# Performance work log

Measured on AMD Instinct MI355X. Metric: run time of the kernel, lower is better.

Reference implementation:

```python
import jax, jax.numpy as jnp
import numpy as np

NDIM = 2
NSIG = 2
NCELLS = 1000
BATCH = 4
DT = 1e-3
NSTEPS = 251  # 1 + int((t1 - t0)/dt) with t0=0, t1=0.25
SIGMA = 1e-3


def _phi(y, pw1, pb1, pw2, pb2, pw3, pb3, pw4, pb4, pw5, pb5):
    # phi_nn: 2 -> 16 -> 32 -> 32 -> 16 -> 1 with tanh activations
    h = jnp.tanh(y @ pw1.T + pb1)
    h = jnp.tanh(h @ pw2.T + pb2)
    h = jnp.tanh(h @ pw3.T + pb3)
    h = jnp.tanh(h @ pw4.T + pb4)
    return h @ pw5.T + pb5  # (ncells, 1)


def setup_inputs() -> dict:
    key = jax.random.key(0)
    ks = jax.random.split(key, 16)
    # x = [t0, t1, y0.flat, tcrit, p0(2), p1(2)] per batch item
    y0 = 0.1 * jax.random.normal(ks[0], (BATCH, NCELLS, NDIM), dtype=jnp.float32)
    t0 = jnp.zeros((BATCH, 1), jnp.float32)
    t1 = jnp.full((BATCH, 1), 0.25, jnp.float32)
    tcrit = jnp.full((BATCH, 1), 0.125, jnp.float32)
    p0 = jax.random.normal(ks[1], (BATCH, 2), dtype=jnp.float32)
    p1 = jax.random.normal(ks[2], (BATCH, 2), dtype=jnp.float32)
    x = jnp.concatenate([t0, t1, y0.reshape(BATCH, -1), tcrit, p0, p1], axis=1)
    # Wiener increments ~ N(0, dt)
    dw = np.sqrt(DT).astype(np.float32) * jax.random.normal(
        ks[3], (BATCH, NSTEPS, NCELLS, NDIM), dtype=jnp.float32)
    # phi_nn weights (torch Linear: weight is (out, in)), init N(0, 0.1), bias 0
    def w(k, o, i):
        return 0.1 * jax.random.normal(k, (o, i), dtype=jnp.float32)
    inp = dict(x=x, dw=dw,
               pw1=w(ks[4], 16, 2), pb1=jnp.zeros(16, jnp.float32),
               pw2=w(ks[5], 32, 16), pb2=jnp.zeros(32, jnp.float32),
               pw3=w(ks[6], 32, 32), pb3=jnp.zeros(32, jnp.float32),
               pw4=w(ks[7], 16, 32), pb4=jnp.zeros(16, jnp.float32),
               pw5=w(ks[8], 1, 16), pb5=jnp.zeros(1, jnp.float32),
               tw=w(ks[9], NDIM, NSIG), tb=jnp.zeros(NDIM, jnp.float32))
    return inp


def reference(x, dw, pw1, pb1, pw2, pb2, pw3, pb3, pw4, pb4, pw5, pb5, tw, tb):
    phi_params = (pw1, pb1, pw2, pb2, pw3, pb3, pw4, pb4, pw5, pb5)
    grad_phi = jax.grad(lambda yy: jnp.sum(_phi(yy, *phi_params)))

    def simulate(xi, dwi):
        t0 = xi[0]
        y0 = xi[2:2 + NCELLS * NDIM].reshape(NCELLS, NDIM)
        ps = xi[2 + NCELLS * NDIM:]
        tcrit, p0, p1 = ps[0], ps[1:3], ps[3:5]
        ts = t0 + DT * jnp.arange(NSTEPS, dtype=xi.dtype)

        def step(y, t_dw):
            t, dwt = t_dw
            sig = jnp.where(t < tcrit, p0, p1)      # step signal f_signal(t, params)
            tilt = sig @ tw.T + tb                  # grad_tilt: (ndim,)
            drift = -(grad_phi(y) + tilt)           # f(t, y)
            y_new = y + drift * DT + SIGMA * dwt    # Euler-Maruyama
            return y_new, None

        y_final, _ = jax.lax.scan(step, y0, (ts, dwi))
        return y_final

    return jax.vmap(simulate)(x, dw)  # (BATCH, NCELLS, NDIM)
```

## Files before the change

kernel.cpp:

```cpp
#include <hip/hip_runtime.h>

#define NDIMC 2
#define NCELLS 1000
#define BATCHSZ 4
#define NSTEPS 251
#define XROW 2007

typedef float v2f __attribute__((ext_vector_type(2)));

__device__ __forceinline__ v2f pfma(v2f w, v2f v, v2f a) {
    return __builtin_elementwise_fma(w, v, a);
}

__device__ __forceinline__ float fast_tanh(float x) {
    float e = __builtin_amdgcn_exp2f(x * 2.885390081777926774f);
    float r = __builtin_amdgcn_rcpf(e + 1.0f);
    return fmaf(-2.0f, r, 1.0f);
}

template<int CTRL>
__device__ __forceinline__ float dpp_mov(float x) {
    return __int_as_float(__builtin_amdgcn_update_dpp(
        0, __float_as_int(x), CTRL, 0xf, 0xf, true));
}
template<int CTRL>
__device__ __forceinline__ float dpp_add(float z) { return z + dpp_mov<CTRL>(z); }

__device__ __forceinline__ float row16_sum(float z) {
    z = dpp_add<0xB1>(z);
    z = dpp_add<0x1B>(z);
    z = dpp_add<0x141>(z);
    z = dpp_add<0x140>(z);
    return z;
}

__device__ __forceinline__ float xor16(float z, bool odd) {
    float t = z, u = z;
    asm("v_permlane16_swap_b32 %0, %1" : "+v"(t), "+v"(u));
    return odd ? t : u;
}

struct G16 { v2f p[8]; };
__device__ __forceinline__ G16 gather16(float z) {
    G16 g;
    const float v0 = z;
    const float v1 = dpp_mov<0x4E>(v0);
    const float v2 = dpp_mov<0x141>(v0);
    const float v3 = dpp_mov<0x141>(v1);
    const float v4 = dpp_mov<0x140>(v0);
    const float v5 = dpp_mov<0x140>(v1);
    const float v6 = dpp_mov<0x140>(v2);
    const float v7 = dpp_mov<0x140>(v3);
    g.p[0] = v2f{v0, dpp_mov<0xB1>(v0)};
    g.p[1] = v2f{v1, dpp_mov<0xB1>(v1)};
    g.p[2] = v2f{v2, dpp_mov<0xB1>(v2)};
    g.p[3] = v2f{v3, dpp_mov<0xB1>(v3)};
    g.p[4] = v2f{v4, dpp_mov<0xB1>(v4)};
    g.p[5] = v2f{v5, dpp_mov<0xB1>(v5)};
    g.p[6] = v2f{v6, dpp_mov<0xB1>(v6)};
    g.p[7] = v2f{v7, dpp_mov<0xB1>(v7)};
    return g;
}

__device__ __forceinline__ float gdot16(const v2f (&w)[8], const G16& g, float bias) {
    v2f a0 = {bias, 0.f}, a1 = {0.f, 0.f}, a2 = {0.f, 0.f}, a3 = {0.f, 0.f};
    a0 = pfma(w[0], g.p[0], a0); a1 = pfma(w[1], g.p[1], a1);
    a2 = pfma(w[2], g.p[2], a2); a3 = pfma(w[3], g.p[3], a3);
    a0 = pfma(w[4], g.p[4], a0); a1 = pfma(w[5], g.p[5], a1);
    a2 = pfma(w[6], g.p[6], a2); a3 = pfma(w[7], g.p[7], a3);
    v2f s = (a0 + a1) + (a2 + a3);
    return s[0] + s[1];
}

__global__ __launch_bounds__(64, 2)
void phinn_sde_kernel(const float* __restrict__ x,   const float* __restrict__ dw,
                      const float* __restrict__ pw1, const float* __restrict__ pb1,
                      const float* __restrict__ pw2, const float* __restrict__ pb2,
                      const float* __restrict__ pw3, const float* __restrict__ pb3,
                      const float* __restrict__ pw4, const float* __restrict__ pb4,
                      const float* __restrict__ pw5, const float* __restrict__ pb5,
                      const float* __restrict__ tw,  const float* __restrict__ tb,
                      float* __restrict__ out)
{
    const int tid  = threadIdx.x;
    const int n    = tid & 31;
    const int s16  = n & 15;
    const int hi   = n >> 4;
    const bool odd = hi;
    const int np   = n ^ 16;
    const int rbk  = hi * 16;
    const int grp  = tid >> 5;
    const int b    = blockIdx.x / (NCELLS / 2);
    const int pair = blockIdx.x % (NCELLS / 2);
    const int cell = pair * 2 + grp;

    const int TAU[8] = {0, 2, 7, 5, 15, 13, 8, 10};

    const float r1a = pw1[s16 * 2 + 0];
    const float r1b = pw1[s16 * 2 + 1];
    const float rb1 = pb1[s16];
    const float rb2 = pb2[n];
    const float rb3 = pb3[n];
    const float rb4 = pb4[s16];
    const float rw5 = pw5[s16];

    v2f w2f[8], w3P[8], w3Q[8], w4f[8], w4b[8], w3bP[8], w3bQ[8], w2b[8];
    #pragma unroll
    for (int t = 0; t < 8; ++t) {
        const int j0 = s16 ^ TAU[t];
        const int j1 = j0 ^ 1;
        const int k0 = rbk + j0;
        const int k1 = rbk + j1;
        w2f[t]  = v2f{pw2[n * 16 + j0],   pw2[n * 16 + j1]};
        w3P[t]  = v2f{pw3[n * 32 + k0],   pw3[n * 32 + k1]};
        w3Q[t]  = v2f{pw3[np * 32 + k0],  pw3[np * 32 + k1]};
        w4f[t]  = v2f{pw4[s16 * 32 + k0], pw4[s16 * 32 + k1]};
        w4b[t]  = v2f{pw4[j0 * 32 + n],   pw4[j1 * 32 + n]};
        w3bP[t] = v2f{pw3[k0 * 32 + n],   pw3[k1 * 32 + n]};
        w3bQ[t] = v2f{pw3[k0 * 32 + np],  pw3[k1 * 32 + np]};
        w2b[t]  = v2f{pw2[k0 * 16 + s16], pw2[k1 * 16 + s16]};
    }

    const float* xb = x + (size_t)b * XROW;
    const float t0v    = xb[0];
    const float tcritv = xb[2 + NCELLS * NDIMC];
    const float p0x = xb[2003], p0y = xb[2004];
    const float p1x = xb[2005], p1y = xb[2006];
    const float tA0 = fmaf(p0x, tw[0], fmaf(p0y, tw[1], tb[0]));
    const float tA1 = fmaf(p0x, tw[2], fmaf(p0y, tw[3], tb[1]));
    const float tB0 = fmaf(p1x, tw[0], fmaf(p1y, tw[1], tb[0]));
    const float tB1 = fmaf(p1x, tw[2], fmaf(p1y, tw[3], tb[1]));

    float y0 = xb[2 + cell * 2 + 0];
    float y1 = xb[2 + cell * 2 + 1];

    const float* dwb = dw + (size_t)b * NSTEPS * NCELLS * NDIMC
                          + (size_t)pair * 2 * NDIMC;
    int dwoff = grp * NDIMC;

    #pragma unroll 1
    for (int i = 0; i < NSTEPS; ++i) {
        const float2 dwv = *(const float2*)(dwb + dwoff);
        dwoff += NCELLS * NDIMC;
        const float t = t0v + 0.001f * (float)i;

        const float h1 = fast_tanh(fmaf(r1a, y0, fmaf(r1b, y1, rb1)));

        const G16 G1 = gather16(h1);
        const float h2 = fast_tanh(gdot16(w2f, G1, rb2));

        const G16 G2 = gather16(h2);
        const float h3 = fast_tanh(gdot16(w3P, G2, rb3)
                                   + xor16(gdot16(w3Q, G2, 0.f), odd));

        const G16 G3 = gather16(h3);
        const float A4 = gdot16(w4f, G3, 0.f);
        const float h4 = fast_tanh(A4 + xor16(A4, odd) + rb4);

        const float g4p = rw5 * fmaf(-h4, h4, 1.0f);

        const G16 G4 = gather16(g4p);
        const float g3p = gdot16(w4b, G4, 0.f) * fmaf(-h3, h3, 1.0f);

        const G16 G5 = gather16(g3p);
        const float g2p = (gdot16(w3bP, G5, 0.f)
                           + xor16(gdot16(w3bQ, G5, 0.f), odd))
                          * fmaf(-h2, h2, 1.0f);

        const G16 G6 = gather16(g2p);
        const float A1 = gdot16(w2b, G6, 0.f);
        const float g1p = (A1 + xor16(A1, odd)) * fmaf(-h1, h1, 1.0f);

        const float v0 = row16_sum(r1a * g1p);
        const float v1 = row16_sum(r1b * g1p);

        const bool  cnd   = t < tcritv;
        const float tilt0 = cnd ? tA0 : tB0;
        const float tilt1 = cnd ? tA1 : tB1;
        y0 = fmaf(-0.001f, v0 + tilt0, fmaf(0.001f, dwv.x, y0));
        y1 = fmaf(-0.001f, v1 + tilt1, fmaf(0.001f, dwv.y, y1));
    }

    if (n == 0) {
        *(float2*)(out + ((size_t)b * NCELLS + cell) * NDIMC) = make_float2(y0, y1);
    }
}

extern "C" void kernel_launch(void* const* d_in, const int* in_sizes, int n_in,
                              void* d_out, int out_size, void* d_ws, size_t ws_size,
                              hipStream_t stream) {
    const float* x   = (const float*)d_in[0];
    const float* dw  = (const float*)d_in[1];
    const float* pw1 = (const float*)d_in[2];
    const float* pb1 = (const float*)d_in[3];
    const float* pw2 = (const float*)d_in[4];
    const float* pb2 = (const float*)d_in[5];
    const float* pw3 = (const float*)d_in[6];
    const float* pb3 = (const float*)d_in[7];
    const float* pw4 = (const float*)d_in[8];
    const float* pb4 = (const float*)d_in[9];
    const float* pw5 = (const float*)d_in[10];
    const float* pb5 = (const float*)d_in[11];
    const float* tw  = (const float*)d_in[12];
    const float* tb  = (const float*)d_in[13];
    float* out = (float*)d_out;

    dim3 grid(BATCHSZ * NCELLS / 2);
    dim3 block(64);
    phinn_sde_kernel<<<grid, block, 0, stream>>>(x, dw, pw1, pb1, pw2, pb2,
                                                 pw3, pb3, pw4, pb4, pw5, pb5,
                                                 tw, tb, out);
}
```

Before: 302.8 us.

## Exchange 32-wide layer activations through LDS broadcast instead of DPP gathers

The 32-wide layers (h2->h3, h3->h4, and the backward g3p->g2p, g2p->g1p) now stage their activations in shared memory. Each lane computes its full 32-term dot product from wide LDS broadcast reads, replacing the DPP gather trees and the permlane16 swap half-sums. The weights are reorganised into per-lane 16-pair register arrays to match. This removes many DPP moves and cross-half combines, but adds LDS round-trip latency on the serial critical path of every time step. There is no explicit barrier, so correctness relies on the 32 lanes of each group sitting in the same wavefront.

```diff
diff --git a/kernel.cpp b/kernel.cpp
--- a/kernel.cpp
+++ b/kernel.cpp
@@ -7,6 +7,10 @@
 #define XROW 2007
 
 typedef float v2f __attribute__((ext_vector_type(2)));
+typedef float v4f __attribute__((ext_vector_type(4)));
+
+__device__ __forceinline__ v2f vlo(v4f v) { return __builtin_shufflevector(v, v, 0, 1); }
+__device__ __forceinline__ v2f vhi(v4f v) { return __builtin_shufflevector(v, v, 2, 3); }
 
 __device__ __forceinline__ v2f pfma(v2f w, v2f v, v2f a) {
     return __builtin_elementwise_fma(w, v, a);
@@ -17,6 +21,7 @@
     float r = __builtin_amdgcn_rcpf(e + 1.0f);
     return fmaf(-2.0f, r, 1.0f);
 }
+
 
 template<int CTRL>
 __device__ __forceinline__ float dpp_mov(float x) {
@@ -32,12 +37,6 @@
     z = dpp_add<0x141>(z);
     z = dpp_add<0x140>(z);
     return z;
-}
-
-__device__ __forceinline__ float xor16(float z, bool odd) {
-    float t = z, u = z;
-    asm("v_permlane16_swap_b32 %0, %1" : "+v"(t), "+v"(u));
-    return odd ? t : u;
 }
 
 struct G16 { v2f p[8]; };
@@ -72,6 +71,23 @@
     return s[0] + s[1];
 }
 
+__device__ __forceinline__ float pdot32(const v2f (&w)[16], const float* p, float bias) {
+    v2f a0 = {bias, 0.f}, a1 = {0.f, 0.f}, a2 = {0.f, 0.f}, a3 = {0.f, 0.f};
+    #pragma unroll
+    for (int c = 0; c < 2; ++c) {
+        v4f u0 = *(const v4f*)(p + c * 16);
+        v4f u1 = *(const v4f*)(p + c * 16 + 4);
+        v4f u2 = *(const v4f*)(p + c * 16 + 8);
+        v4f u3 = *(const v4f*)(p + c * 16 + 12);
+        a0 = pfma(w[c*8+0], vlo(u0), a0); a1 = pfma(w[c*8+1], vhi(u0), a1);
+        a2 = pfma(w[c*8+2], vlo(u1), a2); a3 = pfma(w[c*8+3], vhi(u1), a3);
+        a0 = pfma(w[c*8+4], vlo(u2), a0); a1 = pfma(w[c*8+5], vhi(u2), a1);
+        a2 = pfma(w[c*8+6], vlo(u3), a2); a3 = pfma(w[c*8+7], vhi(u3), a3);
+    }
+    v2f s = (a0 + a1) + (a2 + a3);
+    return s[0] + s[1];
+}
+
 __global__ __launch_bounds__(64, 2)
 void phinn_sde_kernel(const float* __restrict__ x,   const float* __restrict__ dw,
                       const float* __restrict__ pw1, const float* __restrict__ pb1,
@@ -82,14 +98,12 @@
                       const float* __restrict__ tw,  const float* __restrict__ tb,
                       float* __restrict__ out)
 {
+    __shared__ __align__(16) float sh[2][4][32];
+
     const int tid  = threadIdx.x;
     const int n    = tid & 31;
+    const int grp  = tid >> 5;
     const int s16  = n & 15;
-    const int hi   = n >> 4;
-    const bool odd = hi;
-    const int np   = n ^ 16;
-    const int rbk  = hi * 16;
-    const int grp  = tid >> 5;
     const int b    = blockIdx.x / (NCELLS / 2);
     const int pair = blockIdx.x % (NCELLS / 2);
     const int cell = pair * 2 + grp;
@@ -104,22 +118,32 @@
     const float rb4 = pb4[s16];
     const float rw5 = pw5[s16];
 
-    v2f w2f[8], w3P[8], w3Q[8], w4f[8], w4b[8], w3bP[8], w3bQ[8], w2b[8];
+    v2f w2f[8], w4b[8];
     #pragma unroll
     for (int t = 0; t < 8; ++t) {
         const int j0 = s16 ^ TAU[t];
         const int j1 = j0 ^ 1;
-        const int k0 = rbk + j0;
-        const int k1 = rbk + j1;
-        w2f[t]  = v2f{pw2[n * 16 + j0],   pw2[n * 16 + j1]};
-        w3P[t]  = v2f{pw3[n * 32 + k0],   pw3[n * 32 + k1]};
-        w3Q[t]  = v2f{pw3[np * 32 + k0],  pw3[np * 32 + k1]};
-        w4f[t]  = v2f{pw4[s16 * 32 + k0], pw4[s16 * 32 + k1]};
-        w4b[t]  = v2f{pw4[j0 * 32 + n],   pw4[j1 * 32 + n]};
-        w3bP[t] = v2f{pw3[k0 * 32 + n],   pw3[k1 * 32 + n]};
-        w3bQ[t] = v2f{pw3[k0 * 32 + np],  pw3[k1 * 32 + np]};
-        w2b[t]  = v2f{pw2[k0 * 16 + s16], pw2[k1 * 16 + s16]};
-    }
+        w2f[t] = v2f{pw2[n * 16 + j0], pw2[n * 16 + j1]};
+        w4b[t] = v2f{pw4[j0 * 32 + n], pw4[j1 * 32 + n]};
+    }
+
+    v2f w3p[16];
+    #pragma unroll
+    for (int j = 0; j < 16; ++j) w3p[j] = ((const v2f*)pw3)[n * 16 + j];
+
+    v2f w4p[16];
+    #pragma unroll
+    for (int j = 0; j < 16; ++j) w4p[j] = ((const v2f*)pw4)[s16 * 16 + j];
+
+    v2f w3cp[16];
+    #pragma unroll
+    for (int j = 0; j < 16; ++j)
+        w3cp[j] = v2f{pw3[(2*j) * 32 + n], pw3[(2*j+1) * 32 + n]};
+
+    v2f w2cp[16];
+    #pragma unroll
+    for (int j = 0; j < 16; ++j)
+        w2cp[j] = v2f{pw2[(2*j) * 16 + s16], pw2[(2*j+1) * 16 + s16]};
 
     const float* xb = x + (size_t)b * XROW;
     const float t0v    = xb[0];
@@ -138,6 +162,11 @@
                           + (size_t)pair * 2 * NDIMC;
     int dwoff = grp * NDIMC;
 
+    const float* l0 = &sh[grp][0][0];
+    const float* l1 = &sh[grp][1][0];
+    const float* l2 = &sh[grp][2][0];
+    const float* l3 = &sh[grp][3][0];
+
     #pragma unroll 1
     for (int i = 0; i < NSTEPS; ++i) {
         const float2 dwv = *(const float2*)(dwb + dwoff);
@@ -148,28 +177,23 @@
 
         const G16 G1 = gather16(h1);
         const float h2 = fast_tanh(gdot16(w2f, G1, rb2));
-
-        const G16 G2 = gather16(h2);
-        const float h3 = fast_tanh(gdot16(w3P, G2, rb3)
-                                   + xor16(gdot16(w3Q, G2, 0.f), odd));
-
-        const G16 G3 = gather16(h3);
-        const float A4 = gdot16(w4f, G3, 0.f);
-        const float h4 = fast_tanh(A4 + xor16(A4, odd) + rb4);
+        sh[grp][0][n] = h2;
+
+        const float h3 = fast_tanh(pdot32(w3p, l0, rb3));
+        sh[grp][1][n] = h3;
+
+        const float h4 = fast_tanh(pdot32(w4p, l1, rb4));
 
         const float g4p = rw5 * fmaf(-h4, h4, 1.0f);
 
         const G16 G4 = gather16(g4p);
         const float g3p = gdot16(w4b, G4, 0.f) * fmaf(-h3, h3, 1.0f);
-
-        const G16 G5 = gather16(g3p);
-        const float g2p = (gdot16(w3bP, G5, 0.f)
-                           + xor16(gdot16(w3bQ, G5, 0.f), odd))
-                          * fmaf(-h2, h2, 1.0f);
-
-        const G16 G6 = gather16(g2p);
-        const float A1 = gdot16(w2b, G6, 0.f);
-        const float g1p = (A1 + xor16(A1, odd)) * fmaf(-h1, h1, 1.0f);
+        sh[grp][2][n] = g3p;
+
+        const float g2p = pdot32(w3cp, l2, 0.f) * fmaf(-h2, h2, 1.0f);
+        sh[grp][3][n] = g2p;
+
+        const float g1p = pdot32(w2cp, l3, 0.f) * fmaf(-h1, h1, 1.0f);
 
         const float v0 = row16_sum(r1a * g1p);
         const float v1 = row16_sum(r1b * g1p);
```

Measured after the change: 283.7 us. 1.07x faster.
